# Kernel optimization log

Hardware: AMD Instinct MI355X
Metric: run time of the kernel (lower is better)

Reference implementation:

```python
import jax, jax.numpy as jnp
import numpy as np

B, T, C = 8, 2048, 1024
NEG_INF = -1e38


def setup_inputs() -> dict:
    key = jax.random.key(0)
    ks = jax.random.split(key, 10)
    s = 1.0 / np.sqrt(C)
    return {
        "x": jax.random.normal(ks[0], (B, T, C), jnp.float32),
        "Wk": jax.random.normal(ks[1], (C, C), jnp.float32) * s,
        "Wv": jax.random.normal(ks[2], (C, C), jnp.float32) * s,
        "Wr": jax.random.normal(ks[3], (C, C), jnp.float32) * s,
        "Wo": jax.random.normal(ks[4], (C, C), jnp.float32) * s,
        "time_decay": jax.random.normal(ks[5], (C,), jnp.float32) * 0.5,
        "time_first": jax.random.normal(ks[6], (C,), jnp.float32) * 0.5,
        "time_mix_key": jax.random.uniform(ks[7], (1, 1, C), jnp.float32),
        "time_mix_value": jax.random.uniform(ks[8], (1, 1, C), jnp.float32),
        "time_mix_receptance": jax.random.uniform(ks[9], (1, 1, C), jnp.float32),
    }


def _wkv(k, v, time_decay, time_first):
    # k, v: [B, T, C]; numerically-stabilized exp-sum recurrence over T
    w = -jnp.exp(time_decay)  # [C]
    u = time_first            # [C]

    def step(carry, kv):
        num, den, mx = carry
        kt, vt = kv  # [B, C]
        # output at this step uses u bonus
        m_out = jnp.maximum(mx, kt + u)
        e1 = jnp.exp(mx - m_out)
        e2 = jnp.exp(kt + u - m_out)
        out = (e1 * num + e2 * vt) / (e1 * den + e2)
        # state update with decay w
        m_new = jnp.maximum(mx + w, kt)
        e1 = jnp.exp(mx + w - m_new)
        e2 = jnp.exp(kt - m_new)
        return (e1 * num + e2 * vt, e1 * den + e2, m_new), out

    init = (jnp.zeros((B, C), jnp.float32),
            jnp.zeros((B, C), jnp.float32),
            jnp.full((B, C), NEG_INF, jnp.float32))
    kT = jnp.swapaxes(k, 0, 1)  # [T, B, C]
    vT = jnp.swapaxes(v, 0, 1)
    _, outs = jax.lax.scan(step, init, (kT, vT))
    return jnp.swapaxes(outs, 0, 1)  # [B, T, C]


def reference(x, Wk, Wv, Wr, Wo, time_decay, time_first,
              time_mix_key, time_mix_value, time_mix_receptance):
    # time_shift: prev_x[t] = x[t-1], zero at t=0
    prev_x = jnp.concatenate([jnp.zeros_like(x[:, :1]), x[:, :-1]], axis=1)

    r_in = x * time_mix_receptance + prev_x * (1 - time_mix_receptance)
    k_in = x * time_mix_key + prev_x * (1 - time_mix_key)
    v_in = x * time_mix_value + prev_x * (1 - time_mix_value)

    receptance = jnp.einsum('btc,dc->btd', r_in, Wr)
    key = jnp.einsum('btc,dc->btd', k_in, Wk)
    value = jnp.einsum('btc,dc->btd', v_in, Wv)

    wkv = _wkv(key, value, time_decay, time_first)
    rwkv = jax.nn.sigmoid(receptance) * wkv
    return jnp.einsum('btc,dc->btd', rwkv, Wo)
```

## Files before the change

### kernel.cpp

```cpp
#include <hip/hip_runtime.h>
#include <cstdint>
#include <cstddef>

#define DEVI __device__ __forceinline__

typedef __attribute__((ext_vector_type(8))) short short8;
typedef __attribute__((ext_vector_type(4))) float f32x4;

constexpr int Bc = 8, Tc = 2048, Cc = 1024;
constexpr int WKV_L = 32, WKV_NCH = 64;

DEVI unsigned short f2b(float f) {
  unsigned int u = __float_as_uint(f);
  unsigned int r = (u + 0x7FFFu + ((u >> 16) & 1u)) >> 16;
  return (unsigned short)r;
}
DEVI float b2f(unsigned short u) {
  return __uint_as_float(((unsigned int)u) << 16);
}

DEVI void gload16(const unsigned short* g, unsigned short* l) {
  __builtin_amdgcn_global_load_lds(
      (const __attribute__((address_space(1))) void*)g,
      (__attribute__((address_space(3))) void*)l, 16, 0, 0);
}

#define FENCE() asm volatile("" ::: "memory")

__global__ void convert4_kernel(const float* __restrict__ W0,
                                const float* __restrict__ W1,
                                const float* __restrict__ W2,
                                const float* __restrict__ W3,
                                unsigned short* __restrict__ o0,
                                unsigned short* __restrict__ o1,
                                unsigned short* __restrict__ o2,
                                unsigned short* __restrict__ o3) {
  const int i = blockIdx.x * blockDim.x + threadIdx.x;
  const int s = blockIdx.y;
  const float* in = s == 0 ? W0 : (s == 1 ? W1 : (s == 2 ? W2 : W3));
  unsigned short* out = s == 0 ? o0 : (s == 1 ? o1 : (s == 2 ? o2 : o3));
  const float4 v = ((const float4*)in)[i];
  ushort4 o;
  o.x = f2b(v.x); o.y = f2b(v.y); o.z = f2b(v.z); o.w = f2b(v.w);
  ((ushort4*)out)[i] = o;
}

__global__ void mix3_kernel(const float* __restrict__ x,
                            const float* __restrict__ tmk,
                            const float* __restrict__ tmv,
                            const float* __restrict__ tmr,
                            unsigned short* __restrict__ kin,
                            unsigned short* __restrict__ vin,
                            unsigned short* __restrict__ rin,
                            long n4) {
  long i = (long)blockIdx.x * blockDim.x + threadIdx.x;
  const long stride = (long)gridDim.x * blockDim.x;
  for (; i < n4; i += stride) {
    const long e = i * 4;
    const int c = (int)(e & (Cc - 1));
    const long bt = e >> 10;
    const int t = (int)(bt & (Tc - 1));
    const float4 xv = *(const float4*)(x + e);
    float4 pv = {0.f, 0.f, 0.f, 0.f};
    if (t > 0) pv = *(const float4*)(x + e - Cc);
    const float4 mk = *(const float4*)(tmk + c);
    const float4 mv = *(const float4*)(tmv + c);
    const float4 mr = *(const float4*)(tmr + c);
    const float* xp = (const float*)&xv;
    const float* pp = (const float*)&pv;
    const float* mkp = (const float*)&mk;
    const float* mvp = (const float*)&mv;
    const float* mrp = (const float*)&mr;
    ushort4 ko, vo, ro;
    unsigned short* kop = (unsigned short*)&ko;
    unsigned short* vop = (unsigned short*)&vo;
    unsigned short* rop = (unsigned short*)&ro;
#pragma unroll
    for (int q = 0; q < 4; ++q) {
      kop[q] = f2b(xp[q] * mkp[q] + pp[q] * (1.f - mkp[q]));
      vop[q] = f2b(xp[q] * mvp[q] + pp[q] * (1.f - mvp[q]));
      rop[q] = f2b(xp[q] * mrp[q] + pp[q] * (1.f - mrp[q]));
    }
    *(ushort4*)(kin + e) = ko;
    *(ushort4*)(vin + e) = vo;
    *(ushort4*)(rin + e) = ro;
  }
}

template <typename OutT>
__global__ __launch_bounds__(512, 2)
void gemm256(const unsigned short* __restrict__ A0,
             const unsigned short* __restrict__ W0, OutT* __restrict__ C0,
             const unsigned short* __restrict__ A1,
             const unsigned short* __restrict__ W1, OutT* __restrict__ C1,
             const unsigned short* __restrict__ A2,
             const unsigned short* __restrict__ W2, OutT* __restrict__ C2,
             int K, int N) {
  constexpr int BK = 64;
  __shared__ alignas(16) unsigned short As[2][256 * BK];
  __shared__ alignas(16) unsigned short Bs[2][256 * BK];
  const int z = blockIdx.z;
  const unsigned short* A = z == 0 ? A0 : (z == 1 ? A1 : A2);
  const unsigned short* W = z == 0 ? W0 : (z == 1 ? W1 : W2);
  OutT* C_out = z == 0 ? C0 : (z == 1 ? C1 : C2);
  const int m0 = blockIdx.x * 256;
  const int n0 = blockIdx.y * 256;
  const int tid = threadIdx.x;
  const int lane = tid & 63;
  const int w = tid >> 6;
  const int wm = w >> 2;
  const int wn = w & 3;
  const int fr = lane & 15;
  const int ksl = lane >> 4;

  f32x4 acc[8][4];
#pragma unroll
  for (int i = 0; i < 8; ++i)
#pragma unroll
    for (int j = 0; j < 4; ++j) acc[i][j] = (f32x4){0.f, 0.f, 0.f, 0.f};

#define STAGE(buf, kt)                                                        \
  {                                                                           \
    _Pragma("unroll")                                                         \
    for (int cc = 0; cc < 4; ++cc) {                                          \
      const int c = w * 256 + cc * 64 + lane;                                 \
      const int row = c >> 3;                                                 \
      const int gsl = (c & 7) ^ (row & 7);                                    \
      gload16(A + (size_t)(m0 + row) * K + (kt) + gsl * 8,                    \
              &As[buf][(w * 256 + cc * 64) * 8]);                             \
      gload16(W + (size_t)(n0 + row) * K + (kt) + gsl * 8,                    \
              &Bs[buf][(w * 256 + cc * 64) * 8]);                             \
    }                                                                         \
  }

#define LDSRD(bufp, row, sl) \
  (*(const short8*)&(bufp)[(row) * 64 + ((((sl) ^ ((row) & 7))) * 8)])

  const int nt = K / BK;
  STAGE(0, 0);
  int cur = 0;
  for (int t = 0; t < nt; ++t) {
    asm volatile("s_waitcnt vmcnt(0)" ::: "memory");
    __builtin_amdgcn_s_barrier();
    FENCE();
    if (t + 1 < nt) STAGE(cur ^ 1, (t + 1) * BK);
    const unsigned short* Ab = As[cur];
    const unsigned short* Bb = Bs[cur];
    const int sl0 = ksl;
    const int sl1 = 4 + ksl;
    short8 a0[4], b0[4], a1g[4], a2g[4], b2[4], a3[4];
#pragma unroll
    for (int i = 0; i < 4; ++i)
      a0[i] = LDSRD(Ab, wm * 128 + i * 16 + fr, sl0);
#pragma unroll
    for (int j = 0; j < 4; ++j)
      b0[j] = LDSRD(Bb, wn * 64 + j * 16 + fr, sl0);
#pragma unroll
    for (int i = 0; i < 4; ++i)
      a1g[i] = LDSRD(Ab, wm * 128 + (4 + i) * 16 + fr, sl0);
#pragma unroll
    for (int i = 0; i < 4; ++i)
#pragma unroll
      for (int j = 0; j < 4; ++j)
        acc[i][j] = __builtin_amdgcn_mfma_f32_16x16x32_bf16(a0[i], b0[j],
                                                            acc[i][j], 0, 0, 0);
#pragma unroll
    for (int i = 0; i < 4; ++i)
      a2g[i] = LDSRD(Ab, wm * 128 + i * 16 + fr, sl1);
#pragma unroll
    for (int j = 0; j < 4; ++j)
      b2[j] = LDSRD(Bb, wn * 64 + j * 16 + fr, sl1);
#pragma unroll
    for (int i = 0; i < 4; ++i)
#pragma unroll
      for (int j = 0; j < 4; ++j)
        acc[4 + i][j] = __builtin_amdgcn_mfma_f32_16x16x32_bf16(a1g[i], b0[j],
                                                                acc[4 + i][j], 0, 0, 0);
#pragma unroll
    for (int i = 0; i < 4; ++i)
      a3[i] = LDSRD(Ab, wm * 128 + (4 + i) * 16 + fr, sl1);
#pragma unroll
    for (int i = 0; i < 4; ++i)
#pragma unroll
      for (int j = 0; j < 4; ++j)
        acc[i][j] = __builtin_amdgcn_mfma_f32_16x16x32_bf16(a2g[i], b2[j],
                                                            acc[i][j], 0, 0, 0);
#pragma unroll
    for (int i = 0; i < 4; ++i)
#pragma unroll
      for (int j = 0; j < 4; ++j)
        acc[4 + i][j] = __builtin_amdgcn_mfma_f32_16x16x32_bf16(a3[i], b2[j],
                                                                acc[4 + i][j], 0, 0, 0);
    FENCE();
    cur ^= 1;
  }
#undef STAGE
#undef LDSRD

  const int orow = (lane >> 4) * 4;
  const int ocol = lane & 15;
#pragma unroll
  for (int i = 0; i < 8; ++i)
#pragma unroll
    for (int j = 0; j < 4; ++j) {
      const size_t rbase = (size_t)(m0 + wm * 128 + i * 16 + orow);
      const int cb = n0 + wn * 64 + j * 16 + ocol;
#pragma unroll
      for (int q = 0; q < 4; ++q) {
        const float vq = acc[i][j][q];
        if constexpr (sizeof(OutT) == 2)
          C_out[(rbase + q) * N + cb] = (OutT)f2b(vq);
        else
          C_out[(rbase + q) * N + cb] = (OutT)vq;
      }
    }
}

__global__ void wkv_phase1(const unsigned short* __restrict__ keyb,
                           const unsigned short* __restrict__ valb,
                           const float* __restrict__ td,
                           float* __restrict__ s_num,
                           float* __restrict__ s_den,
                           float* __restrict__ s_mx) {
  const int g = blockIdx.x * blockDim.x + threadIdx.x;
  const int c = g & (Cc - 1);
  const int j = (g / Cc) & (WKV_NCH - 1);
  const int b = g / (Cc * WKV_NCH);
  const float w = -__expf(td[c]);
  float num = 0.f, den = 0.f, mx = -1e38f;
  size_t idx = ((size_t)b * Tc + (size_t)j * WKV_L) * Cc + c;
#pragma unroll 4
  for (int i = 0; i < WKV_L; ++i, idx += Cc) {
    const float kt = b2f(keyb[idx]);
    const float vt = b2f(valb[idx]);
    const float mw = mx + w;
    const bool cg = mw >= kt;
    const float d = __expf(cg ? kt - mw : mw - kt);
    const float a1 = cg ? 1.f : d;
    const float a2 = cg ? d : 1.f;
    num = a1 * num + a2 * vt;
    den = a1 * den + a2;
    mx = cg ? mw : kt;
  }
  s_num[g] = num; s_den[g] = den; s_mx[g] = mx;
}

__global__ void wkv_phase2(const float* __restrict__ td,
                           float* __restrict__ s_num,
                           float* __restrict__ s_den,
                           float* __restrict__ s_mx) {
  const int g = blockIdx.x * blockDim.x + threadIdx.x;
  const int c = g & (Cc - 1);
  const int b = g / Cc;
  const float Lw = -__expf(td[c]) * (float)WKV_L;
  float num = 0.f, den = 0.f, mx = -1e38f;
  size_t base = (size_t)b * WKV_NCH * Cc + c;
  for (int j = 0; j < WKV_NCH; ++j) {
    const size_t s = base + (size_t)j * Cc;
    const float ln = s_num[s], ld = s_den[s], lm = s_mx[s];
    s_num[s] = num; s_den[s] = den; s_mx[s] = mx;
    const float md = mx + Lw;
    const bool cg = md >= lm;
    const float d = __expf(cg ? lm - md : md - lm);
    const float e1 = cg ? 1.f : d;
    const float e2 = cg ? d : 1.f;
    num = e1 * num + e2 * ln;
    den = e1 * den + e2 * ld;
    mx = cg ? md : lm;
  }
}

__global__ void wkv_phase3(const unsigned short* __restrict__ keyb,
                           const unsigned short* __restrict__ valb,
                           const unsigned short* __restrict__ recb,
                           const float* __restrict__ td,
                           const float* __restrict__ tf,
                           const float* __restrict__ s_num,
                           const float* __restrict__ s_den,
                           const float* __restrict__ s_mx,
                           unsigned short* __restrict__ rwkv) {
  const int g = blockIdx.x * blockDim.x + threadIdx.x;
  const int c = g & (Cc - 1);
  const int j = (g / Cc) & (WKV_NCH - 1);
  const int b = g / (Cc * WKV_NCH);
  const float w = -__expf(td[c]);
  const float u = tf[c];
  float num = s_num[g], den = s_den[g], mx = s_mx[g];
  size_t idx = ((size_t)b * Tc + (size_t)j * WKV_L) * Cc + c;
#pragma unroll 2
  for (int i = 0; i < WKV_L; ++i, idx += Cc) {
    const float kt = b2f(keyb[idx]);
    const float vt = b2f(valb[idx]);
    const float rt = b2f(recb[idx]);
    const float ku = kt + u;
    const bool co = mx >= ku;
    const float dd = __expf(co ? ku - mx : mx - ku);
    const float e1 = co ? 1.f : dd;
    const float e2 = co ? dd : 1.f;
    const float out = (e1 * num + e2 * vt) / (e1 * den + e2);
    const float sr = 1.f / (1.f + __expf(-rt));
    rwkv[idx] = f2b(sr * out);
    const float mw = mx + w;
    const bool cg = mw >= kt;
    const float du = __expf(cg ? kt - mw : mw - kt);
    const float a1 = cg ? 1.f : du;
    const float a2 = cg ? du : 1.f;
    num = a1 * num + a2 * vt;
    den = a1 * den + a2;
    mx = cg ? mw : kt;
  }
}

extern "C" void kernel_launch(void* const* d_in, const int* in_sizes, int n_in,
                              void* d_out, int out_size, void* d_ws, size_t ws_size,
                              hipStream_t stream) {
  const float* x   = (const float*)d_in[0];
  const float* Wk  = (const float*)d_in[1];
  const float* Wv  = (const float*)d_in[2];
  const float* Wr  = (const float*)d_in[3];
  const float* Wo  = (const float*)d_in[4];
  const float* td  = (const float*)d_in[5];
  const float* tf  = (const float*)d_in[6];
  const float* tmk = (const float*)d_in[7];
  const float* tmv = (const float*)d_in[8];
  const float* tmr = (const float*)d_in[9];

  const long BT = (long)Bc * Tc;
  const long NE = BT * Cc;
  const long CC = (long)Cc * Cc;

  char* p = (char*)d_ws;
  unsigned short* Wk_b = (unsigned short*)p; p += CC * 2;
  unsigned short* Wv_b = (unsigned short*)p; p += CC * 2;
  unsigned short* Wr_b = (unsigned short*)p; p += CC * 2;
  unsigned short* Wo_b = (unsigned short*)p; p += CC * 2;
  unsigned short* kin  = (unsigned short*)p; p += NE * 2;
  unsigned short* vin  = (unsigned short*)p; p += NE * 2;
  unsigned short* rin  = (unsigned short*)p; p += NE * 2;
  unsigned short* keyb = (unsigned short*)p; p += NE * 2;
  unsigned short* valb = (unsigned short*)p; p += NE * 2;
  unsigned short* recb = (unsigned short*)p; p += NE * 2;
  unsigned short* rwkv = kin;
  const long NS = (long)Bc * WKV_NCH * Cc;
  float* s_num = (float*)vin;
  float* s_den = s_num + NS;
  float* s_mx  = s_den + NS;

  {
    dim3 g((unsigned)(CC / 4 / 256), 4), b_(256);
    convert4_kernel<<<g, b_, 0, stream>>>(Wk, Wv, Wr, Wo,
                                          Wk_b, Wv_b, Wr_b, Wo_b);
  }

  mix3_kernel<<<2048, 256, 0, stream>>>(x, tmk, tmv, tmr, kin, vin, rin, NE / 4);

  {
    dim3 grid((unsigned)(BT / 256), (unsigned)(Cc / 256), 3), blk(512);
    gemm256<unsigned short><<<grid, blk, 0, stream>>>(
        kin, Wk_b, keyb, vin, Wv_b, valb, rin, Wr_b, recb, Cc, Cc);
  }

  wkv_phase1<<<2048, 256, 0, stream>>>(keyb, valb, td, s_num, s_den, s_mx);
  wkv_phase2<<<32, 256, 0, stream>>>(td, s_num, s_den, s_mx);
  wkv_phase3<<<2048, 256, 0, stream>>>(keyb, valb, recb, td, tf,
                                       s_num, s_den, s_mx, rwkv);

  {
    dim3 grid((unsigned)(BT / 256), (unsigned)(Cc / 256), 1), blk(512);
    gemm256<float><<<grid, blk, 0, stream>>>(
        rwkv, Wo_b, (float*)d_out, rwkv, Wo_b, (float*)d_out,
        rwkv, Wo_b, (float*)d_out, Cc, Cc);
  }
}
```

Measured before the change: 267.8 us.

## Shrink GEMM tiles to 128x128 with 4 waves and fuse prep kernels

Replaces the 256x256, 512-thread GEMM with a 128x128, 256-thread version using a 2x2 wave grid and a simpler two-step K inner loop. This quadruples the block count, spreading work across more CUs and cutting per-thread accumulator registers. The cost is lower data reuse per tile, so more global and LDS traffic per FLOP. It also merges the weight bf16 conversion and token-mix kernels into one launch to save launch overhead.

```diff
diff --git a/kernel.cpp b/kernel.cpp
--- a/kernel.cpp
+++ b/kernel.cpp
@@ -27,34 +27,36 @@
 
 #define FENCE() asm volatile("" ::: "memory")
 
-__global__ void convert4_kernel(const float* __restrict__ W0,
-                                const float* __restrict__ W1,
-                                const float* __restrict__ W2,
-                                const float* __restrict__ W3,
-                                unsigned short* __restrict__ o0,
-                                unsigned short* __restrict__ o1,
-                                unsigned short* __restrict__ o2,
-                                unsigned short* __restrict__ o3) {
-  const int i = blockIdx.x * blockDim.x + threadIdx.x;
-  const int s = blockIdx.y;
-  const float* in = s == 0 ? W0 : (s == 1 ? W1 : (s == 2 ? W2 : W3));
-  unsigned short* out = s == 0 ? o0 : (s == 1 ? o1 : (s == 2 ? o2 : o3));
-  const float4 v = ((const float4*)in)[i];
-  ushort4 o;
-  o.x = f2b(v.x); o.y = f2b(v.y); o.z = f2b(v.z); o.w = f2b(v.w);
-  ((ushort4*)out)[i] = o;
-}
-
-__global__ void mix3_kernel(const float* __restrict__ x,
+__global__ void prep_kernel(const float* __restrict__ x,
+                            const float* __restrict__ Wk,
+                            const float* __restrict__ Wv,
+                            const float* __restrict__ Wr,
+                            const float* __restrict__ Wo,
                             const float* __restrict__ tmk,
                             const float* __restrict__ tmv,
                             const float* __restrict__ tmr,
+                            unsigned short* __restrict__ Wk_b,
+                            unsigned short* __restrict__ Wv_b,
+                            unsigned short* __restrict__ Wr_b,
+                            unsigned short* __restrict__ Wo_b,
                             unsigned short* __restrict__ kin,
                             unsigned short* __restrict__ vin,
-                            unsigned short* __restrict__ rin,
-                            long n4) {
-  long i = (long)blockIdx.x * blockDim.x + threadIdx.x;
-  const long stride = (long)gridDim.x * blockDim.x;
+                            unsigned short* __restrict__ rin) {
+  const int bid = blockIdx.x;
+  if (bid < 4096) {
+    const int s = bid >> 10;
+    const float* in = s == 0 ? Wk : (s == 1 ? Wv : (s == 2 ? Wr : Wo));
+    unsigned short* out = s == 0 ? Wk_b : (s == 1 ? Wv_b : (s == 2 ? Wr_b : Wo_b));
+    const int i = (bid & 1023) * 256 + threadIdx.x;
+    const float4 v = ((const float4*)in)[i];
+    ushort4 o;
+    o.x = f2b(v.x); o.y = f2b(v.y); o.z = f2b(v.z); o.w = f2b(v.w);
+    ((ushort4*)out)[i] = o;
+    return;
+  }
+  const long n4 = (long)Bc * Tc * Cc / 4;
+  long i = (long)(bid - 4096) * 256 + threadIdx.x;
+  const long stride = 2048L * 256;
   for (; i < n4; i += stride) {
     const long e = i * 4;
     const int c = (int)(e & (Cc - 1));
@@ -88,8 +90,8 @@
 }
 
 template <typename OutT>
-__global__ __launch_bounds__(512, 2)
-void gemm256(const unsigned short* __restrict__ A0,
+__global__ __launch_bounds__(256, 2)
+void gemm128(const unsigned short* __restrict__ A0,
              const unsigned short* __restrict__ W0, OutT* __restrict__ C0,
              const unsigned short* __restrict__ A1,
              const unsigned short* __restrict__ W1, OutT* __restrict__ C1,
@@ -97,25 +99,24 @@
              const unsigned short* __restrict__ W2, OutT* __restrict__ C2,
              int K, int N) {
   constexpr int BK = 64;
-  __shared__ alignas(16) unsigned short As[2][256 * BK];
-  __shared__ alignas(16) unsigned short Bs[2][256 * BK];
+  __shared__ alignas(16) unsigned short As[2][128 * BK];
+  __shared__ alignas(16) unsigned short Bs[2][128 * BK];
   const int z = blockIdx.z;
   const unsigned short* A = z == 0 ? A0 : (z == 1 ? A1 : A2);
   const unsigned short* W = z == 0 ? W0 : (z == 1 ? W1 : W2);
   OutT* C_out = z == 0 ? C0 : (z == 1 ? C1 : C2);
-  const int m0 = blockIdx.x * 256;
-  const int n0 = blockIdx.y * 256;
+  const int m0 = blockIdx.x * 128;
+  const int n0 = blockIdx.y * 128;
   const int tid = threadIdx.x;
   const int lane = tid & 63;
   const int w = tid >> 6;
-  const int wm = w >> 2;
-  const int wn = w & 3;
+  const int wr = w >> 1, wc = w & 1;
   const int fr = lane & 15;
   const int ksl = lane >> 4;
 
-  f32x4 acc[8][4];
-#pragma unroll
-  for (int i = 0; i < 8; ++i)
+  f32x4 acc[4][4];
+#pragma unroll
+  for (int i = 0; i < 4; ++i)
 #pragma unroll
     for (int j = 0; j < 4; ++j) acc[i][j] = (f32x4){0.f, 0.f, 0.f, 0.f};
 
@@ -123,13 +124,13 @@
   {                                                                           \
     _Pragma("unroll")                                                         \
     for (int cc = 0; cc < 4; ++cc) {                                          \
-      const int c = w * 256 + cc * 64 + lane;                                 \
+      const int c = cc * 256 + tid;                                           \
       const int row = c >> 3;                                                 \
       const int gsl = (c & 7) ^ (row & 7);                                    \
       gload16(A + (size_t)(m0 + row) * K + (kt) + gsl * 8,                    \
-              &As[buf][(w * 256 + cc * 64) * 8]);                             \
+              &As[buf][(size_t)(cc * 256 + (tid & ~63)) * 8]);                \
       gload16(W + (size_t)(n0 + row) * K + (kt) + gsl * 8,                    \
-              &Bs[buf][(w * 256 + cc * 64) * 8]);                             \
+              &Bs[buf][(size_t)(cc * 256 + (tid & ~63)) * 8]);                \
     }                                                                         \
   }
 
@@ -146,51 +147,23 @@
     if (t + 1 < nt) STAGE(cur ^ 1, (t + 1) * BK);
     const unsigned short* Ab = As[cur];
     const unsigned short* Bb = Bs[cur];
-    const int sl0 = ksl;
-    const int sl1 = 4 + ksl;
-    short8 a0[4], b0[4], a1g[4], a2g[4], b2[4], a3[4];
-#pragma unroll
-    for (int i = 0; i < 4; ++i)
-      a0[i] = LDSRD(Ab, wm * 128 + i * 16 + fr, sl0);
-#pragma unroll
-    for (int j = 0; j < 4; ++j)
-      b0[j] = LDSRD(Bb, wn * 64 + j * 16 + fr, sl0);
-#pragma unroll
-    for (int i = 0; i < 4; ++i)
-      a1g[i] = LDSRD(Ab, wm * 128 + (4 + i) * 16 + fr, sl0);
-#pragma unroll
-    for (int i = 0; i < 4; ++i)
+#pragma unroll
+    for (int ks = 0; ks < 2; ++ks) {
+      const int sl = ks * 4 + ksl;
+      short8 af[4], bf[4];
+#pragma unroll
+      for (int i = 0; i < 4; ++i)
+        af[i] = LDSRD(Ab, wr * 64 + i * 16 + fr, sl);
 #pragma unroll
       for (int j = 0; j < 4; ++j)
-        acc[i][j] = __builtin_amdgcn_mfma_f32_16x16x32_bf16(a0[i], b0[j],
-                                                            acc[i][j], 0, 0, 0);
-#pragma unroll
-    for (int i = 0; i < 4; ++i)
-      a2g[i] = LDSRD(Ab, wm * 128 + i * 16 + fr, sl1);
-#pragma unroll
-    for (int j = 0; j < 4; ++j)
-      b2[j] = LDSRD(Bb, wn * 64 + j * 16 + fr, sl1);
-#pragma unroll
-    for (int i = 0; i < 4; ++i)
-#pragma unroll
-      for (int j = 0; j < 4; ++j)
-        acc[4 + i][j] = __builtin_amdgcn_mfma_f32_16x16x32_bf16(a1g[i], b0[j],
-                                                                acc[4 + i][j], 0, 0, 0);
-#pragma unroll
-    for (int i = 0; i < 4; ++i)
-      a3[i] = LDSRD(Ab, wm * 128 + (4 + i) * 16 + fr, sl1);
-#pragma unroll
-    for (int i = 0; i < 4; ++i)
-#pragma unroll
-      for (int j = 0; j < 4; ++j)
-        acc[i][j] = __builtin_amdgcn_mfma_f32_16x16x32_bf16(a2g[i], b2[j],
-                                                            acc[i][j], 0, 0, 0);
-#pragma unroll
-    for (int i = 0; i < 4; ++i)
-#pragma unroll
-      for (int j = 0; j < 4; ++j)
-        acc[4 + i][j] = __builtin_amdgcn_mfma_f32_16x16x32_bf16(a3[i], b2[j],
-                                                                acc[4 + i][j], 0, 0, 0);
+        bf[j] = LDSRD(Bb, wc * 64 + j * 16 + fr, sl);
+#pragma unroll
+      for (int i = 0; i < 4; ++i)
+#pragma unroll
+        for (int j = 0; j < 4; ++j)
+          acc[i][j] = __builtin_amdgcn_mfma_f32_16x16x32_bf16(af[i], bf[j],
+                                                              acc[i][j], 0, 0, 0);
+    }
     FENCE();
     cur ^= 1;
   }
@@ -200,11 +173,11 @@
   const int orow = (lane >> 4) * 4;
   const int ocol = lane & 15;
 #pragma unroll
-  for (int i = 0; i < 8; ++i)
+  for (int i = 0; i < 4; ++i)
 #pragma unroll
     for (int j = 0; j < 4; ++j) {
-      const size_t rbase = (size_t)(m0 + wm * 128 + i * 16 + orow);
-      const int cb = n0 + wn * 64 + j * 16 + ocol;
+      const size_t rbase = (size_t)(m0 + wr * 64 + i * 16 + orow);
+      const int cb = n0 + wc * 64 + j * 16 + ocol;
 #pragma unroll
       for (int q = 0; q < 4; ++q) {
         const float vq = acc[i][j][q];
@@ -346,17 +319,12 @@
   float* s_den = s_num + NS;
   float* s_mx  = s_den + NS;
 
+  prep_kernel<<<6144, 256, 0, stream>>>(x, Wk, Wv, Wr, Wo, tmk, tmv, tmr,
+                                        Wk_b, Wv_b, Wr_b, Wo_b, kin, vin, rin);
+
   {
-    dim3 g((unsigned)(CC / 4 / 256), 4), b_(256);
-    convert4_kernel<<<g, b_, 0, stream>>>(Wk, Wv, Wr, Wo,
-                                          Wk_b, Wv_b, Wr_b, Wo_b);
-  }
-
-  mix3_kernel<<<2048, 256, 0, stream>>>(x, tmk, tmv, tmr, kin, vin, rin, NE / 4);
-
-  {
-    dim3 grid((unsigned)(BT / 256), (unsigned)(Cc / 256), 3), blk(512);
-    gemm256<unsigned short><<<grid, blk, 0, stream>>>(
+    dim3 grid((unsigned)(BT / 128), (unsigned)(Cc / 128), 3), blk(256);
+    gemm128<unsigned short><<<grid, blk, 0, stream>>>(
         kin, Wk_b, keyb, vin, Wv_b, valb, rin, Wr_b, recb, Cc, Cc);
   }
 
@@ -366,8 +334,8 @@
                                        s_num, s_den, s_mx, rwkv);
 
   {
-    dim3 grid((unsigned)(BT / 256), (unsigned)(Cc / 256), 1), blk(512);
-    gemm256<float><<<grid, blk, 0, stream>>>(
+    dim3 grid((unsigned)(BT / 128), (unsigned)(Cc / 128), 1), blk(256);
+    gemm128<float><<<grid, blk, 0, stream>>>(
         rwkv, Wo_b, (float*)d_out, rwkv, Wo_b, (float*)d_out,
         rwkv, Wo_b, (float*)d_out, Cc, Cc);
   }
```

Measured after the change: 291.5 us. 8.9% more time.
